# Optimization experiments

Hardware: AMD Instinct MI355X
Metric: run time of the kernel (lower is better)

The kernel has to match this reference:

```python
import jax, jax.numpy as jnp
import numpy as np

B, T, EMB, H = 8, 1024, 128, 8


def setup_inputs() -> dict:
    key = jax.random.key(0)
    ks = jax.random.split(key, 7)
    s = 0.02
    return {
        "x": jax.random.normal(ks[0], (B, T, EMB), dtype=jnp.float32),
        "mask": jax.random.randint(ks[1], (1, T, T), 0, 2, dtype=jnp.int32),
        "Wk": (jax.random.normal(ks[2], (EMB * H, EMB), dtype=jnp.float32) * s),
        "Wq": (jax.random.normal(ks[3], (EMB * H, EMB), dtype=jnp.float32) * s),
        "Wv": (jax.random.normal(ks[4], (EMB * H, EMB), dtype=jnp.float32) * s),
        "Wu": (jax.random.normal(ks[5], (EMB, EMB * H), dtype=jnp.float32) * s),
        "bu": (jax.random.normal(ks[6], (EMB,), dtype=jnp.float32) * s),
    }


def reference(x, mask, Wk, Wq, Wv, Wu, bu):
    b, t, e = x.shape  # e == emb; per-head dim also == emb in this module
    h = Wk.shape[0] // e
    # projections: (b,t,e) @ (e, h*e) -> (b,t,h,e) -> (b,h,t,e)
    q = (x @ Wq.T).reshape(b, t, h, e).transpose(0, 2, 1, 3)
    k = (x @ Wk.T).reshape(b, t, h, e).transpose(0, 2, 1, 3)
    v = (x @ Wv.T).reshape(b, t, h, e).transpose(0, 2, 1, 3)
    scale = e ** 0.25  # torch scales q and k each by e**(1/4)
    dot = jnp.einsum('bhqe,bhke->bhqk', q / scale, k / scale)
    # causal mask: strictly-upper triangle (offset=1) set to -inf FIRST
    causal = jnp.triu(jnp.ones((t, t), dtype=bool), k=1)
    dot = jnp.where(causal, -jnp.inf, dot)
    # padding mask: where mask==0 set to -1e9 (overwrites -inf where overlapping)
    dot = jnp.where(mask[:, None] == 0, jnp.float32(-1e9), dot)
    attn = jax.nn.softmax(dot, axis=-1)
    out = jnp.einsum('bhqk,bhke->bhqe', attn, v)
    out = out.transpose(0, 2, 1, 3).reshape(b, t, h * e)
    return out @ Wu.T + bu
```

## Files before the change

### kernel.cpp

```cpp
#include <hip/hip_runtime.h>

#define Bn 8
#define Hn 8
#define Tn 1024
#define Dn 128

typedef __attribute__((ext_vector_type(8))) short bf16x8;
typedef __attribute__((ext_vector_type(4))) float f32x4;

typedef __attribute__((address_space(3))) unsigned int lds_as_t;
typedef __attribute__((address_space(1))) const unsigned int glb_as_t;

static __device__ __forceinline__ void gload_lds16(const unsigned short* g, unsigned short* l) {
    __builtin_amdgcn_global_load_lds((glb_as_t*)g, (lds_as_t*)l, 16, 0, 0);
}
static __device__ __forceinline__ void gload_lds16b(const char* g, char* l) {
    __builtin_amdgcn_global_load_lds((glb_as_t*)g, (lds_as_t*)l, 16, 0, 0);
}

static __device__ __forceinline__ unsigned short f2bf(float f) {
    union { float f; unsigned int u; } v; v.f = f;
    unsigned int u = v.u;
    return (unsigned short)((u + 0x7FFFu + ((u >> 16) & 1u)) >> 16);
}
static __device__ __forceinline__ int pack_bf16(float lo, float hi) {
    return ((int)f2bf(hi) << 16) | (int)f2bf(lo);
}

__global__ __launch_bounds__(256) void prep_kernel(
    const float* __restrict__ x,  const float* __restrict__ Wq,
    const float* __restrict__ Wk, const float* __restrict__ Wv,
    const float* __restrict__ Wu, const int* __restrict__ mask,
    unsigned short* __restrict__ xb,  unsigned short* __restrict__ wqB,
    unsigned short* __restrict__ wkB, unsigned short* __restrict__ wvB,
    unsigned short* __restrict__ wuB, unsigned long long* __restrict__ bits)
{
    const int blk = blockIdx.x;
    const int tid = threadIdx.x;

    if (blk < 1408) {
        const float* in; unsigned short* out; int i4;
        if (blk < 1024)      { in = x;  out = xb;  i4 = blk * 256 + tid; }
        else if (blk < 1152) { in = Wq; out = wqB; i4 = (blk - 1024) * 256 + tid; }
        else if (blk < 1280) { in = Wk; out = wkB; i4 = (blk - 1152) * 256 + tid; }
        else                 { in = Wv; out = wvB; i4 = (blk - 1280) * 256 + tid; }
        float4 f = ((const float4*)in)[i4];
        ushort4 o;
        o.x = f2bf(f.x); o.y = f2bf(f.y); o.z = f2bf(f.z); o.w = f2bf(f.w);
        int base = i4 * 4;
        int row = base >> 7, col = base & 127;
        int scol = (((col >> 3) ^ (row & 15)) << 3) | (col & 7);
        *(ushort4*)(out + row * 128 + scol) = o;
    } else if (blk < 1536) {
        int i4 = (blk - 1408) * 256 + tid;
        float4 f = ((const float4*)Wu)[i4];
        ushort4 o;
        o.x = f2bf(f.x); o.y = f2bf(f.y); o.z = f2bf(f.z); o.w = f2bf(f.w);
        ((ushort4*)wuB)[i4] = o;
    } else {
        int wid  = (blk - 1536) * 4 + (tid >> 6);
        int lane = tid & 63;
#pragma unroll
        for (int i = 0; i < 4; i++) {
            int widx = wid * 4 + i;
            int row = widx >> 4, kt = widx & 15;
            int v = mask[row * Tn + kt * 64 + lane];
            unsigned long long b = __ballot(v != 0);
            if (lane == 0) bits[widx] = b;
        }
    }
}

__global__ __launch_bounds__(256, 2) void qkv_kernel(
    const unsigned short* __restrict__ xb,
    const unsigned short* __restrict__ wqB,
    const unsigned short* __restrict__ wkB,
    const unsigned short* __restrict__ wvB,
    char* __restrict__ Q,
    char* __restrict__ K,
    unsigned short* __restrict__ Vt)
{
    const int bx = blockIdx.x, by = blockIdx.y;
    const int wave = threadIdx.x >> 6;
    const int lane = threadIdx.x & 63;
    const int l16  = lane & 15;
    const int quad = lane >> 4;
    const int wm = wave & 1, wn = wave >> 1;

    __shared__ __align__(16) unsigned short As[128 * 128];
    __shared__ __align__(16) unsigned short Bs[128 * 128];

    const int which = by >> 3;
    const unsigned short* wsel = (which == 0) ? wqB : (which == 1) ? wkB : wvB;
    const unsigned short* Ag = xb + (size_t)bx * 128 * 128;
    const unsigned short* Bg = wsel + (size_t)(by & 7) * 128 * 128;

#pragma unroll
    for (int i = 0; i < 8; i++) {
        int base = (wave * 8 + i) * 512;
        gload_lds16(Ag + base + lane * 8, &As[base]);
        gload_lds16(Bg + base + lane * 8, &Bs[base]);
    }
    __syncthreads();

    bf16x8 a[4][4];
#pragma unroll
    for (int mt = 0; mt < 4; mt++) {
        int row = wm * 64 + mt * 16 + l16;
#pragma unroll
        for (int ks = 0; ks < 4; ks++)
            a[mt][ks] = *(const bf16x8*)(&As[row * 128 + (((ks * 4 + quad) ^ (row & 15)) << 3)]);
    }

    f32x4 acc[4][4];
#pragma unroll
    for (int nt = 0; nt < 4; nt++) {
        int row = wn * 64 + nt * 16 + l16;
        bf16x8 b4[4];
#pragma unroll
        for (int ks = 0; ks < 4; ks++)
            b4[ks] = *(const bf16x8*)(&Bs[row * 128 + (((ks * 4 + quad) ^ (row & 15)) << 3)]);
#pragma unroll
        for (int mt = 0; mt < 4; mt++) {
            f32x4 c = {0.f, 0.f, 0.f, 0.f};
#pragma unroll
            for (int ks = 0; ks < 4; ks++)
                c = __builtin_amdgcn_mfma_f32_16x16x32_bf16(a[mt][ks], b4[ks], c, 0, 0, 0);
            acc[mt][nt] = c;
        }
    }

    const int h_ = by & 7;
    if (which < 2) {
        __syncthreads();
        char* tile = (char*)As;
#pragma unroll
        for (int mt = 0; mt < 4; mt++) {
#pragma unroll
            for (int nt = 0; nt < 4; nt++) {
                int w = __builtin_amdgcn_cvt_pk_fp8_f32(acc[mt][nt][0], acc[mt][nt][1], 0, false);
                w = __builtin_amdgcn_cvt_pk_fp8_f32(acc[mt][nt][2], acc[mt][nt][3], w, true);
                int col = wn * 64 + nt * 16 + l16;
#pragma unroll
                for (int r = 0; r < 4; r++)
                    tile[(wm * 64 + mt * 16 + quad * 4 + r) * 144 + col] = (char)(w >> (8 * r));
            }
        }
        __syncthreads();

        const int f = threadIdx.x;
        int row = f >> 1;
        int t_in = (bx & 7) * 128 + row;
        int b_ = bx >> 3;
        char* dst = (which == 0) ? Q : K;
        size_t rowbase = ((size_t)((b_ * Hn + h_) * Tn + t_in)) * 128;
#pragma unroll
        for (int i = 0; i < 4; i++) {
            int c = (f & 1) * 4 + i;
            int4 v = *(const int4*)(tile + row * 144 + c * 16);
            int cc = (which == 1) ? (c ^ (row & 7)) : c;
            *(int4*)(dst + rowbase + cc * 16) = v;
        }
    } else {
#pragma unroll
        for (int mt = 0; mt < 4; mt++) {
            int m_base = bx * 128 + wm * 64 + mt * 16 + quad * 4;
            int b_ = m_base >> 10;
            int t0 = m_base & 1023;
#pragma unroll
            for (int nt = 0; nt < 4; nt++) {
                int e_ = wn * 64 + nt * 16 + l16;
                int kt_ = t0 >> 6, tc0 = t0 & 63;
                size_t off = ((((size_t)(b_ * Hn + h_) * 16 + kt_) * 128 + e_) << 6)
                           + ((((tc0 >> 3) ^ (e_ & 7)) << 3) | (tc0 & 7));
                ushort4 v4;
                v4.x = f2bf(acc[mt][nt][0]); v4.y = f2bf(acc[mt][nt][1]);
                v4.z = f2bf(acc[mt][nt][2]); v4.w = f2bf(acc[mt][nt][3]);
                *(ushort4*)(Vt + off) = v4;
            }
        }
    }
}

__global__ __launch_bounds__(256, 3) void attn_kernel(
    const char* __restrict__ Q,
    const char* __restrict__ K,
    const unsigned short* __restrict__ Vt,
    const unsigned long long* __restrict__ mbits,
    unsigned short* __restrict__ AO)
{
    const int qt   = 15 - ((blockIdx.x + blockIdx.y) & 15);
    const int bh   = blockIdx.y;
    const int wave = threadIdx.x >> 6;
    const int lane = threadIdx.x & 63;
    const int l16  = lane & 15;
    const int quad = lane >> 4;

    __shared__ __align__(16) char kbuf[2][64 * 128];
    __shared__ __align__(16) unsigned short vbuf[2][128 * 64];

    const char* Qb = Q  + (size_t)bh * Tn * Dn;
    const char* Kb = K  + (size_t)bh * Tn * Dn;
    const unsigned short* Vb = Vt + (size_t)bh * (16 * 128 * 64);

    const int q0 = qt * 64 + wave * 16;
    const int qrow = q0 + quad * 4;
    const unsigned long long* mrowT = mbits + (size_t)(q0 + l16) * 16;
    const unsigned long long* mrow  = mbits + (size_t)qrow * 16;

    long qf[4];
#pragma unroll
    for (int ks = 0; ks < 4; ks++)
        qf[ks] = *(const long*)(Qb + (size_t)(q0 + l16) * 128 + ks * 32 + quad * 8);

    bf16x8 ones;
#pragma unroll
    for (int j = 0; j < 8; j++) ones[j] = (short)0x3F80;

    f32x4 o[8];
#pragma unroll
    for (int et = 0; et < 8; et++) o[et] = (f32x4){0.f, 0.f, 0.f, 0.f};
    f32x4 lacc = {0.f, 0.f, 0.f, 0.f};

    const float SL = 0.12752041570284543f;

    const int idx0 = (l16 << 2) + ((quad & 1) << 7);
    const int idx1 = idx0 + 64;
    const bool hiQ = (quad >> 1) != 0;

#pragma unroll
    for (int i = 0; i < 2; i++) {
        int base = (wave * 2 + i) * 1024;
        gload_lds16b(Kb + base + lane * 16, &kbuf[0][base]);
    }
#pragma unroll
    for (int i = 0; i < 4; i++) {
        int base = (wave * 4 + i) * 512;
        gload_lds16(Vb + base + lane * 8, &vbuf[0][base]);
    }

    for (int kt = 0; kt <= qt; kt++) {
        const int cur = kt & 1;
        __syncthreads();

        if (kt < qt) {
            const char* Kg = Kb + (kt + 1) * (64 * 128);
            const unsigned short* Vg = Vb + (kt + 1) * (128 * 64);
#pragma unroll
            for (int i = 0; i < 2; i++) {
                int base = (wave * 2 + i) * 1024;
                gload_lds16b(Kg + base + lane * 16, &kbuf[cur ^ 1][base]);
            }
#pragma unroll
            for (int i = 0; i < 4; i++) {
                int base = (wave * 4 + i) * 512;
                gload_lds16(Vg + base + lane * 8, &vbuf[cur ^ 1][base]);
            }
        }

        const unsigned long long mw = mrowT[kt];

        f32x4 s[4];
#pragma unroll
        for (int nt = 0; nt < 4; nt++) {
            int row = nt * 16 + l16;
            long a4[4];
#pragma unroll
            for (int ks = 0; ks < 4; ks++) {
                int c = ks * 2 + (quad >> 1);
                a4[ks] = *(const long*)(&kbuf[cur][row * 128 + (((c ^ (row & 7)) << 4) | ((quad & 1) << 3))]);
            }
            f32x4 c = {0.f, 0.f, 0.f, 0.f};
#pragma unroll
            for (int ks = 0; ks < 4; ks++)
                c = __builtin_amdgcn_mfma_f32_16x16x32_fp8_fp8(a4[ks], qf[ks], c, 0, 0, 0);
            s[nt] = c;
        }

        const int kc0 = kt * 64;
        const int qglob = q0 + l16;
        int w[4][2];
#pragma unroll
        for (int nt = 0; nt < 4; nt++) {
            float pv[4];
#pragma unroll
            for (int r = 0; r < 4; r++) {
                int bit = nt * 16 + quad * 4 + r;
                bool live = ((mw >> bit) & 1ULL) && (kc0 + bit <= qglob);
                pv[r] = live ? __builtin_amdgcn_exp2f(s[nt][r] * SL) : 0.f;
            }
            w[nt][0] = pack_bf16(pv[0], pv[1]);
            w[nt][1] = pack_bf16(pv[2], pv[3]);
        }

        bf16x8 pf[2];
#pragma unroll
        for (int k2 = 0; k2 < 2; k2++) {
            union { int i[4]; bf16x8 v; } u;
#pragma unroll
            for (int d = 0; d < 4; d++) {
                int idx = (d < 2) ? idx0 : idx1;
                int va = __builtin_amdgcn_ds_bpermute(idx, w[2 * k2][d & 1]);
                int vb = __builtin_amdgcn_ds_bpermute(idx, w[2 * k2 + 1][d & 1]);
                u.i[d] = hiQ ? vb : va;
            }
            pf[k2] = u.v;
        }

#pragma unroll
        for (int k2 = 0; k2 < 2; k2++)
            lacc = __builtin_amdgcn_mfma_f32_16x16x32_bf16(pf[k2], ones, lacc, 0, 0, 0);

#pragma unroll
        for (int et = 0; et < 8; et++) {
            int row = et * 16 + l16;
#pragma unroll
            for (int k2 = 0; k2 < 2; k2++) {
                bf16x8 b = *(const bf16x8*)(&vbuf[cur][row * 64 + (((k2 * 4 + quad) ^ (l16 & 7)) << 3)]);
                o[et] = __builtin_amdgcn_mfma_f32_16x16x32_bf16(pf[k2], b, o[et], 0, 0, 0);
            }
        }
    }

    __syncthreads();
    {
        bool deg = (lacc[0] == 0.f) | (lacc[1] == 0.f) | (lacc[2] == 0.f) | (lacc[3] == 0.f);
        if (__ballot(deg) != 0ULL) {
            unsigned short* pb = (unsigned short*)((char*)kbuf + wave * 2304);
            unsigned short dsel[4];
#pragma unroll
            for (int r = 0; r < 4; r++) dsel[r] = (lacc[r] == 0.f) ? (unsigned short)0x3F80 : (unsigned short)0;
            for (int kt = 0; kt < 16; kt++) {
                unsigned long long mw2[4];
#pragma unroll
                for (int r = 0; r < 4; r++) mw2[r] = mrow[r * 16 + kt];
#pragma unroll
                for (int nt = 0; nt < 4; nt++) {
                    int bi = nt * 16 + l16;
#pragma unroll
                    for (int r = 0; r < 4; r++)
                        pb[(quad * 4 + r) * 72 + bi] = ((mw2[r] >> bi) & 1ULL) ? (unsigned short)0 : dsel[r];
                }
                bf16x8 pf[2];
#pragma unroll
                for (int k2 = 0; k2 < 2; k2++)
                    pf[k2] = *(const bf16x8*)(&pb[l16 * 72 + k2 * 32 + quad * 8]);
#pragma unroll
                for (int k2 = 0; k2 < 2; k2++)
                    lacc = __builtin_amdgcn_mfma_f32_16x16x32_bf16(pf[k2], ones, lacc, 0, 0, 0);
                const unsigned short* Vg = Vb + kt * (128 * 64);
#pragma unroll
                for (int et = 0; et < 8; et++) {
#pragma unroll
                    for (int k2 = 0; k2 < 2; k2++) {
                        bf16x8 b = *(const bf16x8*)(Vg + (et * 16 + l16) * 64 + (((k2 * 4 + quad) ^ (l16 & 7)) << 3));
                        o[et] = __builtin_amdgcn_mfma_f32_16x16x32_bf16(pf[k2], b, o[et], 0, 0, 0);
                    }
                }
            }
        }
    }

    const int b_ = bh >> 3, h_ = bh & 7;
#pragma unroll
    for (int r = 0; r < 4; r++) {
        float inv = 1.f / lacc[r];
        int q = qrow + r;
        size_t rowoff = (size_t)(b_ * Tn + q) * (Hn * Dn) + h_ * Dn;
#pragma unroll
        for (int et = 0; et < 8; et++)
            AO[rowoff + et * 16 + l16] = f2bf(o[et][r] * inv);
    }
}

__global__ __launch_bounds__(256) void outproj_kernel(
    const unsigned short* __restrict__ AO,
    const unsigned short* __restrict__ wuB,
    const float* __restrict__ bu,
    float* __restrict__ out)
{
    const int wave = threadIdx.x >> 6;
    const int lane = threadIdx.x & 63;
    const int l16  = lane & 15;
    const int quad = lane >> 4;
    const int m0 = blockIdx.x * 32;

    __shared__ float red[4][32][128];

    f32x4 acc[2][8];
#pragma unroll
    for (int ml = 0; ml < 2; ml++)
#pragma unroll
        for (int nt = 0; nt < 8; nt++) acc[ml][nt] = (f32x4){0.f, 0.f, 0.f, 0.f};

    const int kk0 = wave * 8;
#pragma unroll
    for (int g = 0; g < 8; g++) {
        int kk = kk0 + g;
        bf16x8 a0 = *(const bf16x8*)(AO + (size_t)(m0 + l16) * 1024 + kk * 32 + quad * 8);
        bf16x8 a1 = *(const bf16x8*)(AO + (size_t)(m0 + 16 + l16) * 1024 + kk * 32 + quad * 8);
#pragma unroll
        for (int nt = 0; nt < 8; nt++) {
            bf16x8 b = *(const bf16x8*)(wuB + (size_t)(nt * 16 + l16) * 1024 + kk * 32 + quad * 8);
            acc[0][nt] = __builtin_amdgcn_mfma_f32_16x16x32_bf16(a0, b, acc[0][nt], 0, 0, 0);
            acc[1][nt] = __builtin_amdgcn_mfma_f32_16x16x32_bf16(a1, b, acc[1][nt], 0, 0, 0);
        }
    }

#pragma unroll
    for (int ml = 0; ml < 2; ml++)
#pragma unroll
        for (int nt = 0; nt < 8; nt++)
#pragma unroll
            for (int r = 0; r < 4; r++)
                red[wave][ml * 16 + quad * 4 + r][nt * 16 + l16] = acc[ml][nt][r];
    __syncthreads();

#pragma unroll
    for (int i = 0; i < 4; i++) {
        int flat4 = i * 256 + threadIdx.x;
        int row = flat4 >> 5, c4 = (flat4 & 31) * 4;
        f32x4 v = *(const f32x4*)(&red[0][row][c4]);
#pragma unroll
        for (int w = 1; w < 4; w++) {
            f32x4 p = *(const f32x4*)(&red[w][row][c4]);
            v[0] += p[0]; v[1] += p[1]; v[2] += p[2]; v[3] += p[3];
        }
        float4 bb = *(const float4*)(bu + c4);
        v[0] += bb.x; v[1] += bb.y; v[2] += bb.z; v[3] += bb.w;
        *(f32x4*)(out + (size_t)(m0 + row) * Dn + c4) = v;
    }
}

extern "C" void kernel_launch(void* const* d_in, const int* in_sizes, int n_in,
                              void* d_out, int out_size, void* d_ws, size_t ws_size,
                              hipStream_t stream) {
    const float* x   = (const float*)d_in[0];
    const int* mask  = (const int*)d_in[1];
    const float* Wk  = (const float*)d_in[2];
    const float* Wq  = (const float*)d_in[3];
    const float* Wv  = (const float*)d_in[4];
    const float* Wu  = (const float*)d_in[5];
    const float* bu  = (const float*)d_in[6];
    float* out = (float*)d_out;

    char* ws = (char*)d_ws;
    unsigned short* xb  = (unsigned short*)ws; ws += (size_t)8192 * 128 * 2;
    unsigned short* wqB = (unsigned short*)ws; ws += (size_t)1024 * 128 * 2;
    unsigned short* wkB = (unsigned short*)ws; ws += (size_t)1024 * 128 * 2;
    unsigned short* wvB = (unsigned short*)ws; ws += (size_t)1024 * 128 * 2;
    unsigned short* wuB = (unsigned short*)ws; ws += (size_t)128 * 1024 * 2;
    char* Qf  = ws; ws += (size_t)64 * 1024 * 128;
    char* Kf  = ws; ws += (size_t)64 * 1024 * 128;
    unsigned short* Vtw = (unsigned short*)ws; ws += (size_t)64 * 1024 * 128 * 2;
    unsigned short* AOw = (unsigned short*)ws; ws += (size_t)8192 * 1024 * 2;
    unsigned long long* mb = (unsigned long long*)ws; ws += (size_t)1024 * 16 * 8;

    prep_kernel<<<dim3(2560), 256, 0, stream>>>(x, Wq, Wk, Wv, Wu, mask,
                                                xb, wqB, wkB, wvB, wuB, mb);
    qkv_kernel<<<dim3(64, 24), 256, 0, stream>>>(xb, wqB, wkB, wvB, Qf, Kf, Vtw);
    attn_kernel<<<dim3(16, 64), 256, 0, stream>>>(Qf, Kf, Vtw, mb, AOw);
    outproj_kernel<<<dim3(256), 256, 0, stream>>>(AOw, wuB, bu, out);
}
```

Before: 151.5 us.

## Pre-swizzle Wu into MFMA fragment order, transpose mask bits, truncate P packing

Several unrelated changes land together. Wu is converted to bf16 in the exact per-lane MFMA B-fragment order, so the out-projection reads it with fully coalesced 16-byte loads, and that kernel now uses 16-row tiles with twice as many blocks for more parallelism. The mask bitmap is stored key-tile-major, so lanes in a wave read consecutive words. Softmax probabilities are packed to bf16 by truncation with a single byte-permute instead of round-to-nearest, which saves ALU work in the attention inner loop at a small cost in precision.

```diff
diff --git a/kernel.cpp b/kernel.cpp
--- a/kernel.cpp
+++ b/kernel.cpp
@@ -23,8 +23,10 @@
     unsigned int u = v.u;
     return (unsigned short)((u + 0x7FFFu + ((u >> 16) & 1u)) >> 16);
 }
-static __device__ __forceinline__ int pack_bf16(float lo, float hi) {
-    return ((int)f2bf(hi) << 16) | (int)f2bf(lo);
+static __device__ __forceinline__ int pack_bf16_trunc(float lo, float hi) {
+    union { float f; unsigned int u; } a, b;
+    a.f = lo; b.f = hi;
+    return (int)__builtin_amdgcn_perm(b.u, a.u, 0x07060302u);
 }
 
 __global__ __launch_bounds__(256) void prep_kernel(
@@ -33,7 +35,7 @@
     const float* __restrict__ Wu, const int* __restrict__ mask,
     unsigned short* __restrict__ xb,  unsigned short* __restrict__ wqB,
     unsigned short* __restrict__ wkB, unsigned short* __restrict__ wvB,
-    unsigned short* __restrict__ wuB, unsigned long long* __restrict__ bits)
+    unsigned short* __restrict__ wuR, unsigned long long* __restrict__ bits)
 {
     const int blk = blockIdx.x;
     const int tid = threadIdx.x;
@@ -52,11 +54,22 @@
         int scol = (((col >> 3) ^ (row & 15)) << 3) | (col & 7);
         *(ushort4*)(out + row * 128 + scol) = o;
     } else if (blk < 1536) {
-        int i4 = (blk - 1408) * 256 + tid;
-        float4 f = ((const float4*)Wu)[i4];
-        ushort4 o;
-        o.x = f2bf(f.x); o.y = f2bf(f.y); o.z = f2bf(f.z); o.w = f2bf(f.w);
-        ((ushort4*)wuB)[i4] = o;
+        int fid = (blk - 1408) * 128 + tid;
+        if (tid < 128) {
+            int lane_ = fid & 63;
+            int l16_ = lane_ & 15, quad_ = lane_ >> 4;
+            int nt = (fid >> 6) & 7, kk = fid >> 9;
+            int row = nt * 16 + l16_;
+            int col = kk * 32 + quad_ * 8;
+            const float* src = Wu + (size_t)row * 1024 + col;
+            float4 f0 = *(const float4*)(src);
+            float4 f1 = *(const float4*)(src + 4);
+            unsigned short o[8];
+            o[0] = f2bf(f0.x); o[1] = f2bf(f0.y); o[2] = f2bf(f0.z); o[3] = f2bf(f0.w);
+            o[4] = f2bf(f1.x); o[5] = f2bf(f1.y); o[6] = f2bf(f1.z); o[7] = f2bf(f1.w);
+            *(ushort4*)(wuR + (size_t)fid * 8)     = *(ushort4*)&o[0];
+            *(ushort4*)(wuR + (size_t)fid * 8 + 4) = *(ushort4*)&o[4];
+        }
     } else {
         int wid  = (blk - 1536) * 4 + (tid >> 6);
         int lane = tid & 63;
@@ -66,7 +79,7 @@
             int row = widx >> 4, kt = widx & 15;
             int v = mask[row * Tn + kt * 64 + lane];
             unsigned long long b = __ballot(v != 0);
-            if (lane == 0) bits[widx] = b;
+            if (lane == 0) bits[kt * Tn + row] = b;
         }
     }
 }
@@ -205,8 +218,6 @@
 
     const int q0 = qt * 64 + wave * 16;
     const int qrow = q0 + quad * 4;
-    const unsigned long long* mrowT = mbits + (size_t)(q0 + l16) * 16;
-    const unsigned long long* mrow  = mbits + (size_t)qrow * 16;
 
     long qf[4];
 #pragma unroll
@@ -258,7 +269,7 @@
             }
         }
 
-        const unsigned long long mw = mrowT[kt];
+        const unsigned long long mw = mbits[kt * Tn + q0 + l16];
 
         f32x4 s[4];
 #pragma unroll
@@ -289,8 +300,8 @@
                 bool live = ((mw >> bit) & 1ULL) && (kc0 + bit <= qglob);
                 pv[r] = live ? __builtin_amdgcn_exp2f(s[nt][r] * SL) : 0.f;
             }
-            w[nt][0] = pack_bf16(pv[0], pv[1]);
-            w[nt][1] = pack_bf16(pv[2], pv[3]);
+            w[nt][0] = pack_bf16_trunc(pv[0], pv[1]);
+            w[nt][1] = pack_bf16_trunc(pv[2], pv[3]);
         }
 
         bf16x8 pf[2];
@@ -333,7 +344,7 @@
             for (int kt = 0; kt < 16; kt++) {
                 unsigned long long mw2[4];
 #pragma unroll
-                for (int r = 0; r < 4; r++) mw2[r] = mrow[r * 16 + kt];
+                for (int r = 0; r < 4; r++) mw2[r] = mbits[kt * Tn + qrow + r];
 #pragma unroll
                 for (int nt = 0; nt < 4; nt++) {
                     int bi = nt * 16 + l16;
@@ -375,7 +386,7 @@
 
 __global__ __launch_bounds__(256) void outproj_kernel(
     const unsigned short* __restrict__ AO,
-    const unsigned short* __restrict__ wuB,
+    const unsigned short* __restrict__ wuR,
     const float* __restrict__ bu,
     float* __restrict__ out)
 {
@@ -383,43 +394,37 @@
     const int lane = threadIdx.x & 63;
     const int l16  = lane & 15;
     const int quad = lane >> 4;
-    const int m0 = blockIdx.x * 32;
-
-    __shared__ float red[4][32][128];
-
-    f32x4 acc[2][8];
-#pragma unroll
-    for (int ml = 0; ml < 2; ml++)
-#pragma unroll
-        for (int nt = 0; nt < 8; nt++) acc[ml][nt] = (f32x4){0.f, 0.f, 0.f, 0.f};
+    const int m0 = blockIdx.x * 16;
+
+    __shared__ float red[4][16][128];
+
+    f32x4 acc[8];
+#pragma unroll
+    for (int nt = 0; nt < 8; nt++) acc[nt] = (f32x4){0.f, 0.f, 0.f, 0.f};
 
     const int kk0 = wave * 8;
 #pragma unroll
     for (int g = 0; g < 8; g++) {
         int kk = kk0 + g;
-        bf16x8 a0 = *(const bf16x8*)(AO + (size_t)(m0 + l16) * 1024 + kk * 32 + quad * 8);
-        bf16x8 a1 = *(const bf16x8*)(AO + (size_t)(m0 + 16 + l16) * 1024 + kk * 32 + quad * 8);
+        bf16x8 a = *(const bf16x8*)(AO + (size_t)(m0 + l16) * 1024 + kk * 32 + quad * 8);
 #pragma unroll
         for (int nt = 0; nt < 8; nt++) {
-            bf16x8 b = *(const bf16x8*)(wuB + (size_t)(nt * 16 + l16) * 1024 + kk * 32 + quad * 8);
-            acc[0][nt] = __builtin_amdgcn_mfma_f32_16x16x32_bf16(a0, b, acc[0][nt], 0, 0, 0);
-            acc[1][nt] = __builtin_amdgcn_mfma_f32_16x16x32_bf16(a1, b, acc[1][nt], 0, 0, 0);
-        }
-    }
-
-#pragma unroll
-    for (int ml = 0; ml < 2; ml++)
-#pragma unroll
-        for (int nt = 0; nt < 8; nt++)
-#pragma unroll
-            for (int r = 0; r < 4; r++)
-                red[wave][ml * 16 + quad * 4 + r][nt * 16 + l16] = acc[ml][nt][r];
+            bf16x8 b = *(const bf16x8*)(wuR + ((size_t)(kk * 8 + nt) * 64 + lane) * 8);
+            acc[nt] = __builtin_amdgcn_mfma_f32_16x16x32_bf16(a, b, acc[nt], 0, 0, 0);
+        }
+    }
+
+#pragma unroll
+    for (int nt = 0; nt < 8; nt++)
+#pragma unroll
+        for (int r = 0; r < 4; r++)
+            red[wave][quad * 4 + r][nt * 16 + l16] = acc[nt][r];
     __syncthreads();
 
 #pragma unroll
-    for (int i = 0; i < 4; i++) {
-        int flat4 = i * 256 + threadIdx.x;
-        int row = flat4 >> 5, c4 = (flat4 & 31) * 4;
+    for (int i = 0; i < 2; i++) {
+        int flat = threadIdx.x * 2 + i;
+        int row = flat >> 5, c4 = (flat & 31) * 4;
         f32x4 v = *(const f32x4*)(&red[0][row][c4]);
 #pragma unroll
         for (int w = 1; w < 4; w++) {
@@ -449,7 +454,7 @@
     unsigned short* wqB = (unsigned short*)ws; ws += (size_t)1024 * 128 * 2;
     unsigned short* wkB = (unsigned short*)ws; ws += (size_t)1024 * 128 * 2;
     unsigned short* wvB = (unsigned short*)ws; ws += (size_t)1024 * 128 * 2;
-    unsigned short* wuB = (unsigned short*)ws; ws += (size_t)128 * 1024 * 2;
+    unsigned short* wuR = (unsigned short*)ws; ws += (size_t)128 * 1024 * 2;
     char* Qf  = ws; ws += (size_t)64 * 1024 * 128;
     char* Kf  = ws; ws += (size_t)64 * 1024 * 128;
     unsigned short* Vtw = (unsigned short*)ws; ws += (size_t)64 * 1024 * 128 * 2;
@@ -457,8 +462,8 @@
     unsigned long long* mb = (unsigned long long*)ws; ws += (size_t)1024 * 16 * 8;
 
     prep_kernel<<<dim3(2560), 256, 0, stream>>>(x, Wq, Wk, Wv, Wu, mask,
-                                                xb, wqB, wkB, wvB, wuB, mb);
+                                                xb, wqB, wkB, wvB, wuR, mb);
     qkv_kernel<<<dim3(64, 24), 256, 0, stream>>>(xb, wqB, wkB, wvB, Qf, Kf, Vtw);
     attn_kernel<<<dim3(16, 64), 256, 0, stream>>>(Qf, Kf, Vtw, mb, AOw);
-    outproj_kernel<<<dim3(256), 256, 0, stream>>>(AOw, wuB, bu, out);
-}
+    outproj_kernel<<<dim3(512), 256, 0, stream>>>(AOw, wuR, bu, out);
+}
```

Measured after the change: 149.3 us. No clear change (-1.4%).
